# Performance work log

Hardware: AMD Instinct MI355X
Metric: run time of the kernel (lower is better)

## Reference

```python
import jax, jax.numpy as jnp
import numpy as np

P_MASK = 0.2
HALF = (2, 25, 25)            # n_consecutive // 2 for (T, H, W)
NPIX = 5 * 51 * 51            # np.prod(n_consecutive) = 13005


def setup_inputs() -> dict:
    key = jax.random.key(0)
    ks = jax.random.split(key, 10)
    B, T, H, W, C = 4, 32, 224, 224, 3
    N = 2000
    frames = jax.random.normal(ks[0], (B, T, H, W, C), dtype=jnp.float32)
    mask_token = jax.random.normal(ks[1], (C,), dtype=jnp.float32)
    b = jax.random.randint(ks[2], (N,), 0, B)
    t = jax.random.randint(ks[3], (N,), 0, T)
    h = jax.random.randint(ks[4], (N,), 0, H)
    w = jax.random.randint(ks[5], (N,), 0, W)
    rb = jax.random.randint(ks[6], (1,), 0, B)
    rt = jax.random.randint(ks[7], (1,), 0, T)
    rh = jax.random.randint(ks[8], (1,), 0, H)
    rw = jax.random.randint(ks[9], (1,), 0, W)
    return dict(frames=frames, mask_token=mask_token, b=b, t=t, h=h, w=w,
                rb=rb, rt=rt, rh=rh, rw=rw)


def _axis_mask(idx, half, size):
    # [n_box, size] float indicator of max(0, idx-half) <= pos < min(idx+half, size-1)
    lo = jnp.maximum(idx - half, 0)[:, None]
    hi = jnp.minimum(idx + half, size - 1)[:, None]   # torch slice upper bound uses size-1
    pos = jnp.arange(size)[None, :]
    return ((pos >= lo) & (pos < hi)).astype(jnp.float32)


def _box_union(b, t, h, w, B, T, H, W):
    # union of all boxes as a single rank-1-factor contraction (no per-box scatter)
    bi = (jnp.arange(B)[None, :] == b[:, None]).astype(jnp.float32)
    ti = _axis_mask(t, HALF[0], T)
    hi = _axis_mask(h, HALF[1], H)
    wi = _axis_mask(w, HALF[2], W)
    return jnp.einsum('ib,it,ih,iw->bthw', bi, ti, hi, wi) > 0


def reference(frames, mask_token, b, t, h, w, rb, rt, rh, rw):
    B, T, H, W, C = frames.shape
    tnpix = B * T * H * W
    n1 = int(tnpix * P_MASK * 0.8 // NPIX)
    n2 = int(tnpix * P_MASK * 0.1 // NPIX)
    R1 = _box_union(b[:n1], t[:n1], h[:n1], w[:n1], B, T, H, W)
    R2 = _box_union(b[n1:n1 + n2], t[n1:n1 + n2], h[n1:n1 + n2], w[n1:n1 + n2], B, T, H, W)
    R3 = _box_union(b[n1 + n2:n1 + 2 * n2], t[n1 + n2:n1 + 2 * n2],
                    h[n1 + n2:n1 + 2 * n2], w[n1 + n2:n1 + 2 * n2], B, T, H, W)
    random_token = frames[rb[0], rt[0], rh[0], rw[0]]   # [C]
    out = jnp.where(R1[..., None], mask_token, frames)
    out = jnp.where(R2[..., None], random_token, out)
    M = (R1 | R2 | R3).reshape(B, T, -1).any(axis=-1)
    return out, M
```

## Files before the change

### kernel.cpp

```cpp
#include <hip/hip_runtime.h>

namespace {
constexpr int B_ = 4, T_ = 32, H_ = 224, W_ = 224;
constexpr int HW_ = H_ * W_;
constexpr int NPIX_ = B_ * T_ * HW_;
constexpr int N1_ = 79;
constexpr int N2_ = 9;
constexpr int NBOX_RW_ = N1_ + N2_;
constexpr int NBOX_M_  = N1_ + 2 * N2_;
constexpr int HALF_T = 2, HALF_HW = 25;
constexpr int GPT_ = 16;
constexpr int GPR_ = W_ / GPT_;
constexpr int GPS_ = H_ * GPR_;
constexpr int NGRP_ = B_ * T_ * GPS_;
}

__global__ __launch_bounds__(256) void build_masks(
    const float* __restrict__ frames,
    const int* __restrict__ bb, const int* __restrict__ tt,
    const int* __restrict__ hh, const int* __restrict__ ww,
    const int* __restrict__ rb, const int* __restrict__ rt,
    const int* __restrict__ rh, const int* __restrict__ rw,
    unsigned* __restrict__ gmask, float* __restrict__ rtok,
    float* __restrict__ Mout)
{
    __shared__ int4 r1[NBOX_RW_];
    __shared__ int4 r2[N2_];
    __shared__ int c1, c2, c3;
    const int s = blockIdx.x;
    const int tid = threadIdx.x;
    if (tid == 0) { c1 = 0; c2 = 0; c3 = 0; }
    __syncthreads();

    if (s == 0 && tid == 0) {
        long idx = (((long)rb[0] * T_ + rt[0]) * H_ + rh[0]) * W_ + rw[0];
        rtok[0] = frames[idx * 3 + 0];
        rtok[1] = frames[idx * 3 + 1];
        rtok[2] = frames[idx * 3 + 2];
    }

    const int sb = s / T_, st = s % T_;
    if (tid < NBOX_M_) {
        const int i = tid;
        int tlo = max(tt[i] - HALF_T, 0);
        int thi = min(tt[i] + HALF_T, T_ - 1);
        if (bb[i] == sb && st >= tlo && st < thi) {
            if (i >= NBOX_RW_) {
                atomicAdd(&c3, 1);
            } else {
                int4 r;
                r.x = max(hh[i] - HALF_HW, 0);
                r.y = min(hh[i] + HALF_HW, H_ - 1);
                r.z = max(ww[i] - HALF_HW, 0);
                r.w = min(ww[i] + HALF_HW, W_ - 1);
                if (i < N1_) r1[atomicAdd(&c1, 1)] = r;
                else         r2[atomicAdd(&c2, 1)] = r;
            }
        }
    }
    __syncthreads();

    if (tid == 0) Mout[s] = (c1 + c2 + c3) > 0 ? 1.0f : 0.0f;

    const int n1 = c1, n2 = c2;
    for (int g = tid; g < GPS_; g += 256) {
        int h  = g / GPR_;
        int w0 = (g - h * GPR_) * GPT_;
        unsigned m1 = 0, m2 = 0;
        for (int j = 0; j < n1; ++j) {
            int4 r = r1[j];
            if (h >= r.x && h < r.y) {
                int lo = max(r.z - w0, 0), hi = min(r.w - w0, GPT_);
                if (hi > lo) m1 |= ((1u << (hi - lo)) - 1u) << lo;
            }
        }
        for (int j = 0; j < n2; ++j) {
            int4 r = r2[j];
            if (h >= r.x && h < r.y) {
                int lo = max(r.z - w0, 0), hi = min(r.w - w0, GPT_);
                if (hi > lo) m2 |= ((1u << (hi - lo)) - 1u) << lo;
            }
        }
        gmask[s * GPS_ + g] = m1 | (m2 << 16);
    }
}

__global__ __launch_bounds__(256, 4) void apply_mask(
    const float* __restrict__ frames, const float* __restrict__ mtok,
    const unsigned* __restrict__ gmask, const float* __restrict__ rtok,
    float* __restrict__ out)
{
    const int gid = blockIdx.x * 256 + threadIdx.x;
    const unsigned mw = gmask[gid];

    const float4* fin = (const float4*)(frames + (long)gid * (GPT_ * 3));
    float4 f[12];
#pragma unroll
    for (int k = 0; k < 12; ++k) f[k] = fin[k];

    if (mw) {
        float mt0 = mtok[0], mt1 = mtok[1], mt2 = mtok[2];
        float rt0 = rtok[0], rt1 = rtok[1], rt2 = rtok[2];
        unsigned m1 = mw & 0xFFFFu, m2 = mw >> 16;
        float* v = (float*)f;
#pragma unroll
        for (int k = 0; k < GPT_; ++k) {
            bool b2 = (m2 >> k) & 1u, b1 = (m1 >> k) & 1u;
            v[k * 3 + 0] = b2 ? rt0 : (b1 ? mt0 : v[k * 3 + 0]);
            v[k * 3 + 1] = b2 ? rt1 : (b1 ? mt1 : v[k * 3 + 1]);
            v[k * 3 + 2] = b2 ? rt2 : (b1 ? mt2 : v[k * 3 + 2]);
        }
    }

    float4* fo = (float4*)(out + (long)gid * (GPT_ * 3));
#pragma unroll
    for (int k = 0; k < 12; ++k) fo[k] = f[k];
}

extern "C" void kernel_launch(void* const* d_in, const int* in_sizes, int n_in,
                              void* d_out, int out_size, void* d_ws, size_t ws_size,
                              hipStream_t stream)
{
    const float* frames = (const float*)d_in[0];
    const float* mtok   = (const float*)d_in[1];
    const int* b  = (const int*)d_in[2];
    const int* t  = (const int*)d_in[3];
    const int* h  = (const int*)d_in[4];
    const int* w  = (const int*)d_in[5];
    const int* rb = (const int*)d_in[6];
    const int* rt = (const int*)d_in[7];
    const int* rh = (const int*)d_in[8];
    const int* rw = (const int*)d_in[9];

    unsigned* gmask = (unsigned*)d_ws;
    float*    rtok  = (float*)((char*)d_ws + (size_t)NGRP_ * 4);

    float* out_frames = (float*)d_out;
    float* out_M      = out_frames + (long)NPIX_ * 3;

    build_masks<<<B_ * T_, 256, 0, stream>>>(frames, b, t, h, w, rb, rt, rh, rw,
                                             gmask, rtok, out_M);

    apply_mask<<<NGRP_ / 256, 256, 0, stream>>>(frames, mtok, gmask, rtok,
                                                out_frames);
}
```

Baseline: 183.7 us.

## Coalesce apply_mask accesses with block tiles and shared-memory mask lookup

Measured after the change: 170.5 us. -7.2%, faster.

```diff
diff --git a/kernel.cpp b/kernel.cpp
--- a/kernel.cpp
+++ b/kernel.cpp
@@ -13,6 +13,11 @@
 constexpr int GPR_ = W_ / GPT_;
 constexpr int GPS_ = H_ * GPR_;
 constexpr int NGRP_ = B_ * T_ * GPS_;
+constexpr int F4_TOTAL_ = NPIX_ * 3 / 4;
+constexpr int TILE_F4_ = 1536;
+constexpr int TILE_PX_ = 2048;
+constexpr int TILE_W_  = TILE_PX_ / GPT_;
+constexpr int NBLK_ = F4_TOTAL_ / TILE_F4_;
 }
 
 __global__ __launch_bounds__(256) void build_masks(
@@ -85,36 +90,55 @@
     }
 }
 
-__global__ __launch_bounds__(256, 4) void apply_mask(
-    const float* __restrict__ frames, const float* __restrict__ mtok,
+__global__ __launch_bounds__(256) void apply_mask(
+    const float4* __restrict__ frames4, const float* __restrict__ mtok,
     const unsigned* __restrict__ gmask, const float* __restrict__ rtok,
-    float* __restrict__ out)
+    float4* __restrict__ out4)
 {
-    const int gid = blockIdx.x * 256 + threadIdx.x;
-    const unsigned mw = gmask[gid];
+    __shared__ unsigned smask[TILE_W_];
+    __shared__ float stok[6];
+    const int tid = threadIdx.x;
+    const int blk = blockIdx.x;
 
-    const float4* fin = (const float4*)(frames + (long)gid * (GPT_ * 3));
-    float4 f[12];
+    unsigned wv = 0;
+    if (tid < TILE_W_) { wv = gmask[blk * TILE_W_ + tid]; smask[tid] = wv; }
+    if (tid == 0) {
+        stok[0] = mtok[0]; stok[1] = mtok[1]; stok[2] = mtok[2];
+        stok[3] = rtok[0]; stok[4] = rtok[1]; stok[5] = rtok[2];
+    }
+
+    const long ebase = (long)blk * TILE_F4_;
+    float4 f[6];
 #pragma unroll
-    for (int k = 0; k < 12; ++k) f[k] = fin[k];
+    for (int k = 0; k < 6; ++k) f[k] = frames4[ebase + tid + k * 256];
 
-    if (mw) {
-        float mt0 = mtok[0], mt1 = mtok[1], mt2 = mtok[2];
-        float rt0 = rtok[0], rt1 = rtok[1], rt2 = rtok[2];
-        unsigned m1 = mw & 0xFFFFu, m2 = mw >> 16;
-        float* v = (float*)f;
+    const int any = __syncthreads_or(int(wv != 0));
+
+    if (any) {
 #pragma unroll
-        for (int k = 0; k < GPT_; ++k) {
-            bool b2 = (m2 >> k) & 1u, b1 = (m1 >> k) & 1u;
-            v[k * 3 + 0] = b2 ? rt0 : (b1 ? mt0 : v[k * 3 + 0]);
-            v[k * 3 + 1] = b2 ? rt1 : (b1 ? mt1 : v[k * 3 + 1]);
-            v[k * 3 + 2] = b2 ? rt2 : (b1 ? mt2 : v[k * 3 + 2]);
+        for (int k = 0; k < 6; ++k) {
+            const int el = tid + k * 256;
+            const int pl = (4 * el) / 3;
+            const unsigned wa = smask[pl >> 4];
+            const unsigned wb = smask[(pl + 1) >> 4];
+            if (wa | wb) {
+                float* v = (float*)&f[k];
+#pragma unroll
+                for (int j = 0; j < 4; ++j) {
+                    int fi = 4 * el + j;
+                    int q  = fi / 3;
+                    int c  = fi - 3 * q;
+                    unsigned w = smask[q >> 4];
+                    int bpos = q & 15;
+                    if ((w >> (bpos + 16)) & 1u)      v[j] = stok[3 + c];
+                    else if ((w >> bpos) & 1u)        v[j] = stok[c];
+                }
+            }
         }
     }
 
-    float4* fo = (float4*)(out + (long)gid * (GPT_ * 3));
 #pragma unroll
-    for (int k = 0; k < 12; ++k) fo[k] = f[k];
+    for (int k = 0; k < 6; ++k) out4[ebase + tid + k * 256] = f[k];
 }
 
 extern "C" void kernel_launch(void* const* d_in, const int* in_sizes, int n_in,
@@ -141,6 +165,6 @@
     build_masks<<<B_ * T_, 256, 0, stream>>>(frames, b, t, h, w, rb, rt, rh, rw,
                                              gmask, rtok, out_M);
 
-    apply_mask<<<NGRP_ / 256, 256, 0, stream>>>(frames, mtok, gmask, rtok,
-                                                out_frames);
+    apply_mask<<<NBLK_, 256, 0, stream>>>((const float4*)frames, mtok, gmask,
+                                          rtok, (float4*)out_frames);
 }
```

## Rewrite apply_mask as coalesced grid-stride float4 stream with nontemporal stores

Applied to the files above, without the earlier changes.

Result: faster. 167.8 us (-8.7%).

```diff
diff --git a/kernel.cpp b/kernel.cpp
--- a/kernel.cpp
+++ b/kernel.cpp
@@ -13,7 +13,13 @@
 constexpr int GPR_ = W_ / GPT_;
 constexpr int GPS_ = H_ * GPR_;
 constexpr int NGRP_ = B_ * T_ * GPS_;
+constexpr int F4_TOTAL_ = NPIX_ * 3 / 4;
+constexpr int ABLK_ = 2352;
+constexpr unsigned STRIDE_ = ABLK_ * 256;
+constexpr int NITER_ = F4_TOTAL_ / (int)STRIDE_;
 }
+
+typedef float floatx4 __attribute__((ext_vector_type(4)));
 
 __global__ __launch_bounds__(256) void build_masks(
     const float* __restrict__ frames,
@@ -85,36 +91,45 @@
     }
 }
 
-__global__ __launch_bounds__(256, 4) void apply_mask(
-    const float* __restrict__ frames, const float* __restrict__ mtok,
+__global__ __launch_bounds__(256) void apply_mask(
+    const floatx4* __restrict__ frames4, const float* __restrict__ mtok,
     const unsigned* __restrict__ gmask, const float* __restrict__ rtok,
-    float* __restrict__ out)
+    floatx4* __restrict__ out4)
 {
-    const int gid = blockIdx.x * 256 + threadIdx.x;
-    const unsigned mw = gmask[gid];
+    const unsigned tid0 = blockIdx.x * 256u + threadIdx.x;
+    const unsigned ph = tid0 % 3u;
 
-    const float4* fin = (const float4*)(frames + (long)gid * (GPT_ * 3));
-    float4 f[12];
+    float m0 = mtok[0], m1 = mtok[1], m2 = mtok[2];
+    float r0 = rtok[0], r1 = rtok[1], r2 = rtok[2];
+    float a0 = ph == 0 ? m0 : (ph == 1 ? m1 : m2);
+    float a1 = ph == 0 ? m1 : (ph == 1 ? m2 : m0);
+    float a2 = ph == 0 ? m2 : (ph == 1 ? m0 : m1);
+    float b0 = ph == 0 ? r0 : (ph == 1 ? r1 : r2);
+    float b1 = ph == 0 ? r1 : (ph == 1 ? r2 : r0);
+    float b2 = ph == 0 ? r2 : (ph == 1 ? r0 : r1);
+    const unsigned d1 = (ph + 1) / 3, d2 = (ph + 2) / 3;
+
 #pragma unroll
-    for (int k = 0; k < 12; ++k) f[k] = fin[k];
-
-    if (mw) {
-        float mt0 = mtok[0], mt1 = mtok[1], mt2 = mtok[2];
-        float rt0 = rtok[0], rt1 = rtok[1], rt2 = rtok[2];
-        unsigned m1 = mw & 0xFFFFu, m2 = mw >> 16;
-        float* v = (float*)f;
-#pragma unroll
-        for (int k = 0; k < GPT_; ++k) {
-            bool b2 = (m2 >> k) & 1u, b1 = (m1 >> k) & 1u;
-            v[k * 3 + 0] = b2 ? rt0 : (b1 ? mt0 : v[k * 3 + 0]);
-            v[k * 3 + 1] = b2 ? rt1 : (b1 ? mt1 : v[k * 3 + 1]);
-            v[k * 3 + 2] = b2 ? rt2 : (b1 ? mt2 : v[k * 3 + 2]);
+    for (int it = 0; it < NITER_; ++it) {
+        const unsigned g4 = tid0 + (unsigned)it * STRIDE_;
+        const unsigned m = (4u * g4 - ph) * 0xAAAAAAABu;
+        const unsigned w0i = m >> 4;
+        const unsigned wa = gmask[w0i];
+        const unsigned wb = gmask[(m + 1u) >> 4];
+        floatx4 v = frames4[g4];
+        if (wa | wb) {
+            unsigned p1 = m + d1, p2 = m + d2, p3 = m + 1u;
+            unsigned w1 = ((p1 >> 4) == w0i) ? wa : wb;
+            unsigned w2 = ((p2 >> 4) == w0i) ? wa : wb;
+            unsigned w3 = ((p3 >> 4) == w0i) ? wa : wb;
+            unsigned q0 = m & 15u, q1 = p1 & 15u, q2 = p2 & 15u, q3 = p3 & 15u;
+            v.x = ((wa >> (q0 + 16)) & 1u) ? b0 : (((wa >> q0) & 1u) ? a0 : v.x);
+            v.y = ((w1 >> (q1 + 16)) & 1u) ? b1 : (((w1 >> q1) & 1u) ? a1 : v.y);
+            v.z = ((w2 >> (q2 + 16)) & 1u) ? b2 : (((w2 >> q2) & 1u) ? a2 : v.z);
+            v.w = ((w3 >> (q3 + 16)) & 1u) ? b0 : (((w3 >> q3) & 1u) ? a0 : v.w);
         }
+        __builtin_nontemporal_store(v, &out4[g4]);
     }
-
-    float4* fo = (float4*)(out + (long)gid * (GPT_ * 3));
-#pragma unroll
-    for (int k = 0; k < 12; ++k) fo[k] = f[k];
 }
 
 extern "C" void kernel_launch(void* const* d_in, const int* in_sizes, int n_in,
@@ -141,6 +156,6 @@
     build_masks<<<B_ * T_, 256, 0, stream>>>(frames, b, t, h, w, rb, rt, rh, rw,
                                              gmask, rtok, out_M);
 
-    apply_mask<<<NGRP_ / 256, 256, 0, stream>>>(frames, mtok, gmask, rtok,
-                                                out_frames);
+    apply_mask<<<ABLK_, 256, 0, stream>>>((const floatx4*)frames, mtok, gmask,
+                                          rtok, (floatx4*)out_frames);
 }
```

## Replace fused masked copy with device memcpy plus sparse token scatter

Applied to the files above, without the earlier changes.

Result: faster. 173.7 us (-5.4%).

```diff
diff --git a/kernel.cpp b/kernel.cpp
--- a/kernel.cpp
+++ b/kernel.cpp
@@ -14,6 +14,8 @@
 constexpr int GPS_ = H_ * GPR_;
 constexpr int NGRP_ = B_ * T_ * GPS_;
 }
+
+typedef float floatx4 __attribute__((ext_vector_type(4)));
 
 __global__ __launch_bounds__(256) void build_masks(
     const float* __restrict__ frames,
@@ -85,36 +87,43 @@
     }
 }
 
-__global__ __launch_bounds__(256, 4) void apply_mask(
-    const float* __restrict__ frames, const float* __restrict__ mtok,
-    const unsigned* __restrict__ gmask, const float* __restrict__ rtok,
-    float* __restrict__ out)
+__global__ __launch_bounds__(256) void scatter_tokens(
+    const unsigned* __restrict__ gmask, const float* __restrict__ mtok,
+    const float* __restrict__ rtok, float* __restrict__ out)
 {
-    const int gid = blockIdx.x * 256 + threadIdx.x;
-    const unsigned mw = gmask[gid];
+    const int g = blockIdx.x * 256 + threadIdx.x;
+    const unsigned mw = gmask[g];
+    if (!mw) return;
+    const unsigned m1 = mw & 0xFFFFu, m2 = mw >> 16;
+    float* base = out + (long)g * (GPT_ * 3);
 
-    const float4* fin = (const float4*)(frames + (long)gid * (GPT_ * 3));
-    float4 f[12];
+    if ((m2 == 0u && m1 == 0xFFFFu) || m2 == 0xFFFFu) {
+        const float* tk = (m2 == 0xFFFFu) ? rtok : mtok;
+        float t0 = tk[0], t1 = tk[1], t2 = tk[2];
+        floatx4 p0 = {t0, t1, t2, t0};
+        floatx4 p1 = {t1, t2, t0, t1};
+        floatx4 p2 = {t2, t0, t1, t2};
+        floatx4* b4 = (floatx4*)base;
 #pragma unroll
-    for (int k = 0; k < 12; ++k) f[k] = fin[k];
+        for (int i = 0; i < 4; ++i) {
+            b4[3 * i + 0] = p0;
+            b4[3 * i + 1] = p1;
+            b4[3 * i + 2] = p2;
+        }
+        return;
+    }
 
-    if (mw) {
-        float mt0 = mtok[0], mt1 = mtok[1], mt2 = mtok[2];
-        float rt0 = rtok[0], rt1 = rtok[1], rt2 = rtok[2];
-        unsigned m1 = mw & 0xFFFFu, m2 = mw >> 16;
-        float* v = (float*)f;
+    float a0 = mtok[0], a1 = mtok[1], a2 = mtok[2];
+    float b0 = rtok[0], b1 = rtok[1], b2 = rtok[2];
 #pragma unroll
-        for (int k = 0; k < GPT_; ++k) {
-            bool b2 = (m2 >> k) & 1u, b1 = (m1 >> k) & 1u;
-            v[k * 3 + 0] = b2 ? rt0 : (b1 ? mt0 : v[k * 3 + 0]);
-            v[k * 3 + 1] = b2 ? rt1 : (b1 ? mt1 : v[k * 3 + 1]);
-            v[k * 3 + 2] = b2 ? rt2 : (b1 ? mt2 : v[k * 3 + 2]);
+    for (int k = 0; k < GPT_; ++k) {
+        unsigned bit = 1u << k;
+        if (m2 & bit) {
+            base[3 * k + 0] = b0; base[3 * k + 1] = b1; base[3 * k + 2] = b2;
+        } else if (m1 & bit) {
+            base[3 * k + 0] = a0; base[3 * k + 1] = a1; base[3 * k + 2] = a2;
         }
     }
-
-    float4* fo = (float4*)(out + (long)gid * (GPT_ * 3));
-#pragma unroll
-    for (int k = 0; k < 12; ++k) fo[k] = f[k];
 }
 
 extern "C" void kernel_launch(void* const* d_in, const int* in_sizes, int n_in,
@@ -138,9 +147,12 @@
     float* out_frames = (float*)d_out;
     float* out_M      = out_frames + (long)NPIX_ * 3;
 
+    hipMemcpyAsync(out_frames, frames, (size_t)NPIX_ * 3 * sizeof(float),
+                   hipMemcpyDeviceToDevice, stream);
+
     build_masks<<<B_ * T_, 256, 0, stream>>>(frames, b, t, h, w, rb, rt, rh, rw,
                                              gmask, rtok, out_M);
 
-    apply_mask<<<NGRP_ / 256, 256, 0, stream>>>(frames, mtok, gmask, rtok,
-                                                out_frames);
+    scatter_tokens<<<NGRP_ / 256, 256, 0, stream>>>(gmask, mtok, rtok,
+                                                    out_frames);
 }
```
